# Performance work log

Hardware: AMD Instinct MI355X
Metric: run time of the kernel (lower is better)

The kernel has to match this reference:

```python
import jax, jax.numpy as jnp
import numpy as np
import math

D_MODEL = 1024
NUM_HEADS = 16
D_K = D_MODEL // NUM_HEADS


def setup_inputs() -> dict:
    key = jax.random.key(0)
    ks = jax.random.split(key, 5)
    scale = 1.0 / math.sqrt(D_MODEL)
    x = jax.random.normal(ks[0], (2, 2048, D_MODEL), dtype=jnp.float32)
    qkv_w = jax.random.uniform(ks[1], (3 * D_MODEL, D_MODEL), jnp.float32, -scale, scale)
    qkv_b = jax.random.uniform(ks[2], (3 * D_MODEL,), jnp.float32, -scale, scale)
    out_w = jax.random.uniform(ks[3], (D_MODEL, D_MODEL), jnp.float32, -scale, scale)
    out_b = jax.random.uniform(ks[4], (D_MODEL,), jnp.float32, -scale, scale)
    return {"x": x, "qkv_w": qkv_w, "qkv_b": qkv_b, "out_w": out_w, "out_b": out_b}


def reference(x, qkv_w, qkv_b, out_w, out_b):
    B, N, D = x.shape
    # fused QKV projection (torch Linear: x @ W.T + b)
    qkv = x @ qkv_w.T + qkv_b                       # (B, N, 3D)
    qkv = qkv.reshape(B, N, 3, NUM_HEADS, D_K)
    qkv = jnp.transpose(qkv, (2, 0, 3, 1, 4))        # (3, B, H, N, d_k)
    q, k, v = qkv[0], qkv[1], qkv[2]
    attn = jnp.einsum('bhnd,bhmd->bhnm', q, k) / math.sqrt(D_K)  # (B,H,N,N)
    attn = jax.nn.softmax(attn, axis=-1)
    out = jnp.einsum('bhnm,bhmd->bhnd', attn, v)     # (B,H,N,d_k)
    out = jnp.transpose(out, (0, 2, 1, 3)).reshape(B, N, D)
    return out @ out_w.T + out_b
```

## Files before the change

### kernel.cpp

```cpp
#include <hip/hip_runtime.h>
#include <hip/hip_bf16.h>


typedef __bf16 bf16x8 __attribute__((ext_vector_type(8)));
typedef __bf16 bf16x4 __attribute__((ext_vector_type(4)));
typedef short short4v __attribute__((ext_vector_type(4)));
typedef float f32x4 __attribute__((ext_vector_type(4)));

#define QSCALE 0.18033688011112042f

__device__ __forceinline__ unsigned short bfbits(float f) {
    union { __bf16 h; unsigned short u; } cv;
    cv.h = (__bf16)f;
    return cv.u;
}

__device__ __forceinline__ f32x4 mfma16(bf16x4 a, bf16x4 b, f32x4 c) {
#if __has_builtin(__builtin_amdgcn_mfma_f32_16x16x16bf16_1k)
    union { bf16x4 h; short4v s; } ua, ub;
    ua.h = a; ub.h = b;
    return __builtin_amdgcn_mfma_f32_16x16x16bf16_1k(ua.s, ub.s, c, 0, 0, 0);
#else
    f32x4 d = c;
    asm volatile("v_mfma_f32_16x16x16_bf16 %0, %1, %2, %0"
                 : "+v"(d) : "v"(a), "v"(b));
    return d;
#endif
}

__device__ __forceinline__ void gl_lds16(const void* g, void* l) {
    __builtin_amdgcn_global_load_lds(
        (__attribute__((address_space(1))) const unsigned int*)g,
        (__attribute__((address_space(3))) unsigned int*)l, 16, 0, 0);
}

__global__ void cvt_f32_bf16_v4(const float4* __restrict__ src,
                                ushort4* __restrict__ dst, int n4) {
    int i = blockIdx.x * blockDim.x + threadIdx.x;
    int stride = gridDim.x * blockDim.x;
    for (; i < n4; i += stride) {
        float4 f = src[i];
        ushort4 o;
        o.x = bfbits(f.x); o.y = bfbits(f.y); o.z = bfbits(f.z); o.w = bfbits(f.w);
        dst[i] = o;
    }
}

template<int MODE>
__global__ __launch_bounds__(256, 3) void gemm_mfma(
    const unsigned short* __restrict__ A,
    const unsigned short* __restrict__ W,
    const float* __restrict__ bias,
    unsigned short* __restrict__ qo,
    unsigned short* __restrict__ ko,
    unsigned short* __restrict__ vto,
    float* __restrict__ fo) {
    __shared__ __attribute__((aligned(128))) unsigned char smem[32768];
    const int lane = threadIdx.x & 63;
    const int w = threadIdx.x >> 6;
    const int g = lane >> 4, c = lane & 15;
    const int wr = w >> 1, wc = w & 1;
    const int row0 = blockIdx.x * 128;
    const int col0 = blockIdx.y * 128;

    const int rloc = lane >> 3;
    const int csrc = ((lane & 7) ^ rloc) * 8;

    f32x4 acc[4][4] = {};

    for (int kt = 0; kt < 1024; kt += 64) {
        #pragma unroll
        for (int i = 0; i < 4; ++i) {
            const int r = i * 32 + w * 8 + rloc;
            gl_lds16(A + (size_t)(row0 + r) * 1024 + kt + csrc,
                     smem + i * 4096 + w * 1024);
            gl_lds16(W + (size_t)(col0 + r) * 1024 + kt + csrc,
                     smem + 16384 + i * 4096 + w * 1024);
        }
        __syncthreads();

        #pragma unroll
        for (int ks = 0; ks < 2; ++ks) {
            bf16x8 a[4], b[4];
            #pragma unroll
            for (int mi = 0; mi < 4; ++mi) {
                const int r = wr * 64 + mi * 16 + c;
                a[mi] = *(const bf16x8*)(smem + r * 128 + (((ks * 4 + g) ^ (r & 7)) * 16));
            }
            #pragma unroll
            for (int ni = 0; ni < 4; ++ni) {
                const int r = wc * 64 + ni * 16 + c;
                b[ni] = *(const bf16x8*)(smem + 16384 + r * 128 + (((ks * 4 + g) ^ (r & 7)) * 16));
            }
            #pragma unroll
            for (int mi = 0; mi < 4; ++mi)
                #pragma unroll
                for (int ni = 0; ni < 4; ++ni)
                    acc[mi][ni] = __builtin_amdgcn_mfma_f32_16x16x32_bf16(
                        a[mi], b[ni], acc[mi][ni], 0, 0, 0);
        }
        __syncthreads();
    }

    #pragma unroll
    for (int mi = 0; mi < 4; ++mi) {
        #pragma unroll
        for (int ni = 0; ni < 4; ++ni) {
            const int col = col0 + wc * 64 + ni * 16 + c;
            const float bv = bias[col];
            #pragma unroll
            for (int j = 0; j < 4; ++j) {
                const int row = row0 + wr * 64 + mi * 16 + 4 * g + j;
                float v = acc[mi][ni][j] + bv;
                if (MODE == 1) {
                    fo[(size_t)row * 1024 + col] = v;
                } else {
                    const int sec = col >> 10;
                    const int d = col & 1023;
                    const int h = d >> 6, dk = d & 63;
                    const int b_ = row >> 11, n = row & 2047;
                    const int bh = b_ * 16 + h;
                    if (sec == 0)
                        qo[((size_t)(bh * 2048 + n) << 6) + dk] = bfbits(v * QSCALE);
                    else if (sec == 1)
                        ko[((size_t)(bh * 2048 + n) << 6) + dk] = bfbits(v);
                    else
                        vto[(size_t)(bh * 64 + dk) * 2048 + n] = bfbits(v);
                }
            }
        }
    }
}

__global__ __launch_bounds__(256, 4) void attn_flash(
    const unsigned short* __restrict__ Q,
    const unsigned short* __restrict__ K,
    const unsigned short* __restrict__ Vt,
    unsigned short* __restrict__ O) {
    __shared__ __attribute__((aligned(128))) unsigned char smem[32768];
    const int lane = threadIdx.x & 63;
    const int w = threadIdx.x >> 6;
    const int g = lane >> 4, c = lane & 15;
    const int c7 = c & 7;
    const int bh = blockIdx.y;
    const int q0 = blockIdx.x * 64 + w * 16;
    const unsigned short* Qb = Q + (size_t)bh * 2048 * 64;
    const unsigned short* Kb = K + (size_t)bh * 2048 * 64;
    const unsigned short* Vb = Vt + (size_t)bh * 64 * 2048;

    const int rloc = lane >> 3;
    const int csrc = ((lane & 7) ^ (rloc & 7)) * 8;

    const int chunkKV0 = ((0 + g) ^ c7) * 16;
    const int chunkKV1 = ((4 + g) ^ c7) * 16;
    const int ghalf = (g >> 1);
    const int gsub = (g & 1) * 8;

    bf16x8 aq[2];
    #pragma unroll
    for (int ks = 0; ks < 2; ++ks)
        aq[ks] = *(const bf16x8*)(Qb + (size_t)(q0 + c) * 64 + ks * 32 + 8 * g);

    f32x4 o[4] = {};
    f32x4 l_run = {};
    float m_run = -1e30f;

    bf16x4 ones4;
    #pragma unroll
    for (int i = 0; i < 4; ++i) ones4[i] = (__bf16)1.0f;

    #pragma unroll
    for (int tt = 0; tt < 2; ++tt) {
        const int t = 2 * w + tt;
        const int row = 8 * t + rloc;
        gl_lds16(Kb + (size_t)row * 64 + csrc, smem + t * 1024);
        gl_lds16(Vb + (size_t)row * 2048 + csrc, smem + 16384 + t * 1024);
    }
    __syncthreads();

    int cur = 0;
    for (int kv = 0; kv < 2048; kv += 64) {
        if (kv + 64 < 2048) {
            const int nb = cur ^ 1;
            #pragma unroll
            for (int tt = 0; tt < 2; ++tt) {
                const int t = 2 * w + tt;
                const int row = 8 * t + rloc;
                gl_lds16(Kb + (size_t)(kv + 64 + row) * 64 + csrc,
                         smem + nb * 8192 + t * 1024);
                gl_lds16(Vb + (size_t)row * 2048 + (kv + 64) + csrc,
                         smem + 16384 + nb * 8192 + t * 1024);
            }
        }

        const unsigned char* Kt = smem + cur * 8192;
        const unsigned char* Vtb = smem + 16384 + cur * 8192;

        f32x4 s[4] = {};
        __builtin_amdgcn_s_setprio(1);
        #pragma unroll
        for (int nj = 0; nj < 4; ++nj) {
            bf16x8 bk0 = *(const bf16x8*)(Kt + nj * 2048 + c * 128 + chunkKV0);
            bf16x8 bk1 = *(const bf16x8*)(Kt + nj * 2048 + c * 128 + chunkKV1);
            s[nj] = __builtin_amdgcn_mfma_f32_16x16x32_bf16(bk0, aq[0], s[nj], 0, 0, 0);
            s[nj] = __builtin_amdgcn_mfma_f32_16x16x32_bf16(bk1, aq[1], s[nj], 0, 0, 0);
        }
        __builtin_amdgcn_s_setprio(0);

        float pmax = s[0][0];
        #pragma unroll
        for (int nj = 0; nj < 4; ++nj)
            #pragma unroll
            for (int j = 0; j < 4; ++j)
                pmax = fmaxf(pmax, s[nj][j]);

        if (__any((int)(pmax > m_run + 8.f))) {
            float rm = pmax;
            rm = fmaxf(rm, __shfl_xor(rm, 16));
            rm = fmaxf(rm, __shfl_xor(rm, 32));
            const float mnew = fmaxf(m_run, rm);
            const float sc = __builtin_amdgcn_exp2f(m_run - mnew);
            m_run = mnew;
            #pragma unroll
            for (int j = 0; j < 4; ++j) {
                const float scj = __shfl(sc, 4 * g + j);
                l_run[j] *= scj;
                #pragma unroll
                for (int ni = 0; ni < 4; ++ni)
                    o[ni][j] *= scj;
            }
        }

        bf16x4 p[4];
        #pragma unroll
        for (int nj = 0; nj < 4; ++nj)
            #pragma unroll
            for (int j = 0; j < 4; ++j)
                p[nj][j] = (__bf16)__builtin_amdgcn_exp2f(s[nj][j] - m_run);

        f32x4 lt = {};
        __builtin_amdgcn_s_setprio(1);
        #pragma unroll
        for (int nj = 0; nj < 4; ++nj) {
            lt = mfma16(p[nj], ones4, lt);
            #pragma unroll
            for (int ni = 0; ni < 4; ++ni) {
                bf16x4 bv = *(const bf16x4*)(Vtb + (ni * 16 + c) * 128 +
                                             (((2 * nj + ghalf) ^ c7) * 16) + gsub);
                o[ni] = mfma16(p[nj], bv, o[ni]);
            }
        }
        __builtin_amdgcn_s_setprio(0);
        l_run += lt;

        __syncthreads();
        cur ^= 1;
    }

    const int b_ = bh >> 4, h = bh & 15;
    #pragma unroll
    for (int ni = 0; ni < 4; ++ni) {
        #pragma unroll
        for (int j = 0; j < 4; ++j) {
            const int row = b_ * 2048 + q0 + 4 * g + j;
            const int col = h * 64 + ni * 16 + c;
            O[(size_t)row * 1024 + col] = bfbits(o[ni][j] / l_run[j]);
        }
    }
}

extern "C" void kernel_launch(void* const* d_in, const int* in_sizes, int n_in,
                              void* d_out, int out_size, void* d_ws, size_t ws_size,
                              hipStream_t stream) {
    const float* x     = (const float*)d_in[0];
    const float* qkv_w = (const float*)d_in[1];
    const float* qkv_b = (const float*)d_in[2];
    const float* out_w = (const float*)d_in[3];
    const float* out_b = (const float*)d_in[4];
    float* out = (float*)d_out;

    char* ws = (char*)d_ws;
    unsigned short* xb   = (unsigned short*)(ws);
    unsigned short* wqkv = (unsigned short*)(ws + (8u  << 20));
    unsigned short* wout = (unsigned short*)(ws + (14u << 20));
    unsigned short* qb   = (unsigned short*)(ws + (16u << 20));
    unsigned short* kb   = (unsigned short*)(ws + (24u << 20));
    unsigned short* vtb  = (unsigned short*)(ws + (32u << 20));

    cvt_f32_bf16_v4<<<2048, 256, 0, stream>>>((const float4*)x,     (ushort4*)xb,   4096 * 1024 / 4);
    cvt_f32_bf16_v4<<<2048, 256, 0, stream>>>((const float4*)qkv_w, (ushort4*)wqkv, 3072 * 1024 / 4);
    cvt_f32_bf16_v4<<<1024, 256, 0, stream>>>((const float4*)out_w, (ushort4*)wout, 1024 * 1024 / 4);

    gemm_mfma<0><<<dim3(32, 24), 256, 0, stream>>>(xb, wqkv, qkv_b, qb, kb, vtb, nullptr);

    unsigned short* ao = xb;
    attn_flash<<<dim3(32, 32), 256, 0, stream>>>(qb, kb, vtb, ao);

    gemm_mfma<1><<<dim3(32, 8), 256, 0, stream>>>(ao, wout, out_b, nullptr, nullptr, nullptr, out);
}
```

Before: 130.7 us.

## Process two query groups per wave in attention and merge conversion kernels

Each attention wave now computes 32 query rows as two 16-row groups that share every K and V fragment read from LDS. Blocks shrink to 128 threads, and each thread issues twice the async tile loads. This halves LDS traffic per MFMA and amortizes the softmax bookkeeping, at the cost of higher register pressure and fewer waves per block. The three fp32-to-bf16 conversion launches are also merged into one kernel writing the contiguous workspace.

```diff
diff --git a/kernel.cpp b/kernel.cpp
--- a/kernel.cpp
+++ b/kernel.cpp
@@ -34,12 +34,17 @@
         (__attribute__((address_space(3))) unsigned int*)l, 16, 0, 0);
 }
 
-__global__ void cvt_f32_bf16_v4(const float4* __restrict__ src,
-                                ushort4* __restrict__ dst, int n4) {
+__global__ void cvt_all(const float4* __restrict__ x,
+                        const float4* __restrict__ wq,
+                        const float4* __restrict__ wo,
+                        ushort4* __restrict__ dst) {
     int i = blockIdx.x * blockDim.x + threadIdx.x;
-    int stride = gridDim.x * blockDim.x;
-    for (; i < n4; i += stride) {
-        float4 f = src[i];
+    const int stride = gridDim.x * blockDim.x;
+    for (; i < 2097152; i += stride) {
+        float4 f;
+        if (i < 1048576)       f = x[i];
+        else if (i < 1835008)  f = wq[i - 1048576];
+        else                   f = wo[i - 1835008];
         ushort4 o;
         o.x = bfbits(f.x); o.y = bfbits(f.y); o.z = bfbits(f.z); o.w = bfbits(f.w);
         dst[i] = o;
@@ -132,7 +137,7 @@
     }
 }
 
-__global__ __launch_bounds__(256, 4) void attn_flash(
+__global__ __launch_bounds__(128, 2) void attn_flash(
     const unsigned short* __restrict__ Q,
     const unsigned short* __restrict__ K,
     const unsigned short* __restrict__ Vt,
@@ -143,7 +148,7 @@
     const int g = lane >> 4, c = lane & 15;
     const int c7 = c & 7;
     const int bh = blockIdx.y;
-    const int q0 = blockIdx.x * 64 + w * 16;
+    const int q0 = blockIdx.x * 64 + w * 32;
     const unsigned short* Qb = Q + (size_t)bh * 2048 * 64;
     const unsigned short* Kb = K + (size_t)bh * 2048 * 64;
     const unsigned short* Vb = Vt + (size_t)bh * 64 * 2048;
@@ -156,22 +161,24 @@
     const int ghalf = (g >> 1);
     const int gsub = (g & 1) * 8;
 
-    bf16x8 aq[2];
-    #pragma unroll
-    for (int ks = 0; ks < 2; ++ks)
-        aq[ks] = *(const bf16x8*)(Qb + (size_t)(q0 + c) * 64 + ks * 32 + 8 * g);
-
-    f32x4 o[4] = {};
-    f32x4 l_run = {};
-    float m_run = -1e30f;
+    bf16x8 aq[2][2];
+    #pragma unroll
+    for (int qg = 0; qg < 2; ++qg)
+        #pragma unroll
+        for (int ks = 0; ks < 2; ++ks)
+            aq[qg][ks] = *(const bf16x8*)(Qb + (size_t)(q0 + qg * 16 + c) * 64 + ks * 32 + 8 * g);
+
+    f32x4 oa[4] = {}, ob[4] = {};
+    f32x4 la = {}, lb = {};
+    float ma = -1e30f, mb = -1e30f;
 
     bf16x4 ones4;
     #pragma unroll
     for (int i = 0; i < 4; ++i) ones4[i] = (__bf16)1.0f;
 
     #pragma unroll
-    for (int tt = 0; tt < 2; ++tt) {
-        const int t = 2 * w + tt;
+    for (int tt = 0; tt < 4; ++tt) {
+        const int t = 4 * w + tt;
         const int row = 8 * t + rloc;
         gl_lds16(Kb + (size_t)row * 64 + csrc, smem + t * 1024);
         gl_lds16(Vb + (size_t)row * 2048 + csrc, smem + 16384 + t * 1024);
@@ -183,8 +190,8 @@
         if (kv + 64 < 2048) {
             const int nb = cur ^ 1;
             #pragma unroll
-            for (int tt = 0; tt < 2; ++tt) {
-                const int t = 2 * w + tt;
+            for (int tt = 0; tt < 4; ++tt) {
+                const int t = 4 * w + tt;
                 const int row = 8 * t + rloc;
                 gl_lds16(Kb + (size_t)(kv + 64 + row) * 64 + csrc,
                          smem + nb * 8192 + t * 1024);
@@ -196,62 +203,84 @@
         const unsigned char* Kt = smem + cur * 8192;
         const unsigned char* Vtb = smem + 16384 + cur * 8192;
 
-        f32x4 s[4] = {};
+        f32x4 sa[4] = {}, sb[4] = {};
         __builtin_amdgcn_s_setprio(1);
         #pragma unroll
         for (int nj = 0; nj < 4; ++nj) {
             bf16x8 bk0 = *(const bf16x8*)(Kt + nj * 2048 + c * 128 + chunkKV0);
             bf16x8 bk1 = *(const bf16x8*)(Kt + nj * 2048 + c * 128 + chunkKV1);
-            s[nj] = __builtin_amdgcn_mfma_f32_16x16x32_bf16(bk0, aq[0], s[nj], 0, 0, 0);
-            s[nj] = __builtin_amdgcn_mfma_f32_16x16x32_bf16(bk1, aq[1], s[nj], 0, 0, 0);
+            sa[nj] = __builtin_amdgcn_mfma_f32_16x16x32_bf16(bk0, aq[0][0], sa[nj], 0, 0, 0);
+            sa[nj] = __builtin_amdgcn_mfma_f32_16x16x32_bf16(bk1, aq[0][1], sa[nj], 0, 0, 0);
+            sb[nj] = __builtin_amdgcn_mfma_f32_16x16x32_bf16(bk0, aq[1][0], sb[nj], 0, 0, 0);
+            sb[nj] = __builtin_amdgcn_mfma_f32_16x16x32_bf16(bk1, aq[1][1], sb[nj], 0, 0, 0);
         }
         __builtin_amdgcn_s_setprio(0);
 
-        float pmax = s[0][0];
+        float pa = sa[0][0], pb = sb[0][0];
         #pragma unroll
         for (int nj = 0; nj < 4; ++nj)
             #pragma unroll
-            for (int j = 0; j < 4; ++j)
-                pmax = fmaxf(pmax, s[nj][j]);
-
-        if (__any((int)(pmax > m_run + 8.f))) {
-            float rm = pmax;
+            for (int j = 0; j < 4; ++j) {
+                pa = fmaxf(pa, sa[nj][j]);
+                pb = fmaxf(pb, sb[nj][j]);
+            }
+
+        const bool trig = (pa > ma + 8.f) || (pb > mb + 8.f);
+        if (__any((int)trig)) {
+            float rm = pa;
             rm = fmaxf(rm, __shfl_xor(rm, 16));
             rm = fmaxf(rm, __shfl_xor(rm, 32));
-            const float mnew = fmaxf(m_run, rm);
-            const float sc = __builtin_amdgcn_exp2f(m_run - mnew);
-            m_run = mnew;
+            float mnew = fmaxf(ma, rm);
+            float sc = __builtin_amdgcn_exp2f(ma - mnew);
+            ma = mnew;
             #pragma unroll
             for (int j = 0; j < 4; ++j) {
                 const float scj = __shfl(sc, 4 * g + j);
-                l_run[j] *= scj;
+                la[j] *= scj;
                 #pragma unroll
-                for (int ni = 0; ni < 4; ++ni)
-                    o[ni][j] *= scj;
-            }
-        }
-
-        bf16x4 p[4];
+                for (int ni = 0; ni < 4; ++ni) oa[ni][j] *= scj;
+            }
+            rm = pb;
+            rm = fmaxf(rm, __shfl_xor(rm, 16));
+            rm = fmaxf(rm, __shfl_xor(rm, 32));
+            mnew = fmaxf(mb, rm);
+            sc = __builtin_amdgcn_exp2f(mb - mnew);
+            mb = mnew;
+            #pragma unroll
+            for (int j = 0; j < 4; ++j) {
+                const float scj = __shfl(sc, 4 * g + j);
+                lb[j] *= scj;
+                #pragma unroll
+                for (int ni = 0; ni < 4; ++ni) ob[ni][j] *= scj;
+            }
+        }
+
+        bf16x4 qa_[4], qb_[4];
         #pragma unroll
         for (int nj = 0; nj < 4; ++nj)
             #pragma unroll
-            for (int j = 0; j < 4; ++j)
-                p[nj][j] = (__bf16)__builtin_amdgcn_exp2f(s[nj][j] - m_run);
-
-        f32x4 lt = {};
+            for (int j = 0; j < 4; ++j) {
+                qa_[nj][j] = (__bf16)__builtin_amdgcn_exp2f(sa[nj][j] - ma);
+                qb_[nj][j] = (__bf16)__builtin_amdgcn_exp2f(sb[nj][j] - mb);
+            }
+
+        f32x4 lta = {}, ltb = {};
         __builtin_amdgcn_s_setprio(1);
         #pragma unroll
         for (int nj = 0; nj < 4; ++nj) {
-            lt = mfma16(p[nj], ones4, lt);
+            lta = mfma16(qa_[nj], ones4, lta);
+            ltb = mfma16(qb_[nj], ones4, ltb);
             #pragma unroll
             for (int ni = 0; ni < 4; ++ni) {
                 bf16x4 bv = *(const bf16x4*)(Vtb + (ni * 16 + c) * 128 +
                                              (((2 * nj + ghalf) ^ c7) * 16) + gsub);
-                o[ni] = mfma16(p[nj], bv, o[ni]);
+                oa[ni] = mfma16(qa_[nj], bv, oa[ni]);
+                ob[ni] = mfma16(qb_[nj], bv, ob[ni]);
             }
         }
         __builtin_amdgcn_s_setprio(0);
-        l_run += lt;
+        la += lta;
+        lb += ltb;
 
         __syncthreads();
         cur ^= 1;
@@ -262,9 +291,11 @@
     for (int ni = 0; ni < 4; ++ni) {
         #pragma unroll
         for (int j = 0; j < 4; ++j) {
-            const int row = b_ * 2048 + q0 + 4 * g + j;
             const int col = h * 64 + ni * 16 + c;
-            O[(size_t)row * 1024 + col] = bfbits(o[ni][j] / l_run[j]);
+            const int rowa = b_ * 2048 + q0 + 4 * g + j;
+            O[(size_t)rowa * 1024 + col] = bfbits(oa[ni][j] / la[j]);
+            const int rowb = rowa + 16;
+            O[(size_t)rowb * 1024 + col] = bfbits(ob[ni][j] / lb[j]);
         }
     }
 }
@@ -287,14 +318,13 @@
     unsigned short* kb   = (unsigned short*)(ws + (24u << 20));
     unsigned short* vtb  = (unsigned short*)(ws + (32u << 20));
 
-    cvt_f32_bf16_v4<<<2048, 256, 0, stream>>>((const float4*)x,     (ushort4*)xb,   4096 * 1024 / 4);
-    cvt_f32_bf16_v4<<<2048, 256, 0, stream>>>((const float4*)qkv_w, (ushort4*)wqkv, 3072 * 1024 / 4);
-    cvt_f32_bf16_v4<<<1024, 256, 0, stream>>>((const float4*)out_w, (ushort4*)wout, 1024 * 1024 / 4);
+    cvt_all<<<2048, 256, 0, stream>>>((const float4*)x, (const float4*)qkv_w,
+                                      (const float4*)out_w, (ushort4*)ws);
 
     gemm_mfma<0><<<dim3(32, 24), 256, 0, stream>>>(xb, wqkv, qkv_b, qb, kb, vtb, nullptr);
 
     unsigned short* ao = xb;
-    attn_flash<<<dim3(32, 32), 256, 0, stream>>>(qb, kb, vtb, ao);
+    attn_flash<<<dim3(32, 32), 128, 0, stream>>>(qb, kb, vtb, ao);
 
     gemm_mfma<1><<<dim3(32, 8), 256, 0, stream>>>(ao, wout, out_b, nullptr, nullptr, nullptr, out);
 }
```

Measured after the change: 130.5 us. About the same (-0.2%).

## Software-pipeline attention QK^T with softmax/PV and merge conversion kernels

Applied to the files above, without the earlier changes.

The flash-attention loop is restructured so that the QK^T MFMAs for the next KV tile are issued before the softmax and PV work on the current tile. It uses two score register sets, double-buffered K and triple-buffered V in LDS, which grows LDS from 32 KB to 40 KB. This aims to hide MFMA latency behind the exp/max work and overlap loads further ahead. The three f32-to-bf16 conversion launches are also merged into one kernel over the contiguous workspace, which relies on the fixed buffer offsets.

```diff
diff --git a/kernel.cpp b/kernel.cpp
--- a/kernel.cpp
+++ b/kernel.cpp
@@ -34,12 +34,17 @@
         (__attribute__((address_space(3))) unsigned int*)l, 16, 0, 0);
 }
 
-__global__ void cvt_f32_bf16_v4(const float4* __restrict__ src,
-                                ushort4* __restrict__ dst, int n4) {
+__global__ void cvt_all(const float4* __restrict__ x,
+                        const float4* __restrict__ wq,
+                        const float4* __restrict__ wo,
+                        ushort4* __restrict__ dst) {
     int i = blockIdx.x * blockDim.x + threadIdx.x;
-    int stride = gridDim.x * blockDim.x;
-    for (; i < n4; i += stride) {
-        float4 f = src[i];
+    const int stride = gridDim.x * blockDim.x;
+    for (; i < 2097152; i += stride) {
+        float4 f;
+        if (i < 1048576)       f = x[i];
+        else if (i < 1835008)  f = wq[i - 1048576];
+        else                   f = wo[i - 1835008];
         ushort4 o;
         o.x = bfbits(f.x); o.y = bfbits(f.y); o.z = bfbits(f.z); o.w = bfbits(f.w);
         dst[i] = o;
@@ -137,7 +142,7 @@
     const unsigned short* __restrict__ K,
     const unsigned short* __restrict__ Vt,
     unsigned short* __restrict__ O) {
-    __shared__ __attribute__((aligned(128))) unsigned char smem[32768];
+    __shared__ __attribute__((aligned(128))) unsigned char smem[40960];
     const int lane = threadIdx.x & 63;
     const int w = threadIdx.x >> 6;
     const int g = lane >> 4, c = lane & 15;
@@ -169,93 +174,108 @@
     #pragma unroll
     for (int i = 0; i < 4; ++i) ones4[i] = (__bf16)1.0f;
 
-    #pragma unroll
-    for (int tt = 0; tt < 2; ++tt) {
-        const int t = 2 * w + tt;
-        const int row = 8 * t + rloc;
-        gl_lds16(Kb + (size_t)row * 64 + csrc, smem + t * 1024);
-        gl_lds16(Vb + (size_t)row * 2048 + csrc, smem + 16384 + t * 1024);
-    }
+    #define STAGE(U, KBUF, VBUF)                                               \
+        {                                                                      \
+            _Pragma("unroll")                                                  \
+            for (int tt = 0; tt < 2; ++tt) {                                   \
+                const int t = 2 * w + tt;                                      \
+                const int row = 8 * t + rloc;                                  \
+                gl_lds16(Kb + (size_t)((U) * 64 + row) * 64 + csrc,            \
+                         smem + (KBUF) * 8192 + t * 1024);                     \
+                gl_lds16(Vb + (size_t)row * 2048 + (U) * 64 + csrc,            \
+                         smem + 16384 + (VBUF) * 8192 + t * 1024);             \
+            }                                                                  \
+        }
+
+    #define QKT(S, KBUF)                                                       \
+        {                                                                      \
+            const unsigned char* Kt = smem + (KBUF) * 8192;                    \
+            __builtin_amdgcn_s_setprio(1);                                     \
+            _Pragma("unroll")                                                  \
+            for (int nj = 0; nj < 4; ++nj) {                                   \
+                bf16x8 bk0 = *(const bf16x8*)(Kt + nj * 2048 + c * 128 + chunkKV0); \
+                bf16x8 bk1 = *(const bf16x8*)(Kt + nj * 2048 + c * 128 + chunkKV1); \
+                S[nj] = __builtin_amdgcn_mfma_f32_16x16x32_bf16(bk0, aq[0], S[nj], 0, 0, 0); \
+                S[nj] = __builtin_amdgcn_mfma_f32_16x16x32_bf16(bk1, aq[1], S[nj], 0, 0, 0); \
+            }                                                                  \
+            __builtin_amdgcn_s_setprio(0);                                     \
+        }
+
+    #define SMPV(S, VBUF)                                                      \
+        {                                                                      \
+            float pmax = S[0][0];                                              \
+            _Pragma("unroll")                                                  \
+            for (int nj = 0; nj < 4; ++nj)                                     \
+                _Pragma("unroll")                                              \
+                for (int j = 0; j < 4; ++j)                                    \
+                    pmax = fmaxf(pmax, S[nj][j]);                              \
+            if (__any((int)(pmax > m_run + 8.f))) {                            \
+                float rm = pmax;                                               \
+                rm = fmaxf(rm, __shfl_xor(rm, 16));                            \
+                rm = fmaxf(rm, __shfl_xor(rm, 32));                            \
+                const float mnew = fmaxf(m_run, rm);                           \
+                const float sc = __builtin_amdgcn_exp2f(m_run - mnew);         \
+                m_run = mnew;                                                  \
+                _Pragma("unroll")                                              \
+                for (int j = 0; j < 4; ++j) {                                  \
+                    const float scj = __shfl(sc, 4 * g + j);                   \
+                    l_run[j] *= scj;                                           \
+                    _Pragma("unroll")                                          \
+                    for (int ni = 0; ni < 4; ++ni) o[ni][j] *= scj;            \
+                }                                                              \
+            }                                                                  \
+            bf16x4 p[4];                                                       \
+            _Pragma("unroll")                                                  \
+            for (int nj = 0; nj < 4; ++nj)                                     \
+                _Pragma("unroll")                                              \
+                for (int j = 0; j < 4; ++j)                                    \
+                    p[nj][j] = (__bf16)__builtin_amdgcn_exp2f(S[nj][j] - m_run); \
+            const unsigned char* Vtb = smem + 16384 + (VBUF) * 8192;           \
+            f32x4 lt = {};                                                     \
+            __builtin_amdgcn_s_setprio(1);                                     \
+            _Pragma("unroll")                                                  \
+            for (int nj = 0; nj < 4; ++nj) {                                   \
+                lt = mfma16(p[nj], ones4, lt);                                 \
+                _Pragma("unroll")                                              \
+                for (int ni = 0; ni < 4; ++ni) {                               \
+                    bf16x4 bv = *(const bf16x4*)(Vtb + (ni * 16 + c) * 128 +   \
+                                 (((2 * nj + ghalf) ^ c7) * 16) + gsub);       \
+                    o[ni] = mfma16(p[nj], bv, o[ni]);                          \
+                }                                                              \
+            }                                                                  \
+            __builtin_amdgcn_s_setprio(0);                                     \
+            l_run += lt;                                                       \
+        }
+
+    f32x4 sA[4] = {}, sB[4] = {};
+
+    STAGE(0, 0, 0);
     __syncthreads();
-
-    int cur = 0;
-    for (int kv = 0; kv < 2048; kv += 64) {
-        if (kv + 64 < 2048) {
-            const int nb = cur ^ 1;
-            #pragma unroll
-            for (int tt = 0; tt < 2; ++tt) {
-                const int t = 2 * w + tt;
-                const int row = 8 * t + rloc;
-                gl_lds16(Kb + (size_t)(kv + 64 + row) * 64 + csrc,
-                         smem + nb * 8192 + t * 1024);
-                gl_lds16(Vb + (size_t)row * 2048 + (kv + 64) + csrc,
-                         smem + 16384 + nb * 8192 + t * 1024);
-            }
-        }
-
-        const unsigned char* Kt = smem + cur * 8192;
-        const unsigned char* Vtb = smem + 16384 + cur * 8192;
-
-        f32x4 s[4] = {};
-        __builtin_amdgcn_s_setprio(1);
-        #pragma unroll
-        for (int nj = 0; nj < 4; ++nj) {
-            bf16x8 bk0 = *(const bf16x8*)(Kt + nj * 2048 + c * 128 + chunkKV0);
-            bf16x8 bk1 = *(const bf16x8*)(Kt + nj * 2048 + c * 128 + chunkKV1);
-            s[nj] = __builtin_amdgcn_mfma_f32_16x16x32_bf16(bk0, aq[0], s[nj], 0, 0, 0);
-            s[nj] = __builtin_amdgcn_mfma_f32_16x16x32_bf16(bk1, aq[1], s[nj], 0, 0, 0);
-        }
-        __builtin_amdgcn_s_setprio(0);
-
-        float pmax = s[0][0];
-        #pragma unroll
-        for (int nj = 0; nj < 4; ++nj)
-            #pragma unroll
-            for (int j = 0; j < 4; ++j)
-                pmax = fmaxf(pmax, s[nj][j]);
-
-        if (__any((int)(pmax > m_run + 8.f))) {
-            float rm = pmax;
-            rm = fmaxf(rm, __shfl_xor(rm, 16));
-            rm = fmaxf(rm, __shfl_xor(rm, 32));
-            const float mnew = fmaxf(m_run, rm);
-            const float sc = __builtin_amdgcn_exp2f(m_run - mnew);
-            m_run = mnew;
-            #pragma unroll
-            for (int j = 0; j < 4; ++j) {
-                const float scj = __shfl(sc, 4 * g + j);
-                l_run[j] *= scj;
-                #pragma unroll
-                for (int ni = 0; ni < 4; ++ni)
-                    o[ni][j] *= scj;
-            }
-        }
-
-        bf16x4 p[4];
-        #pragma unroll
-        for (int nj = 0; nj < 4; ++nj)
-            #pragma unroll
-            for (int j = 0; j < 4; ++j)
-                p[nj][j] = (__bf16)__builtin_amdgcn_exp2f(s[nj][j] - m_run);
-
-        f32x4 lt = {};
-        __builtin_amdgcn_s_setprio(1);
-        #pragma unroll
-        for (int nj = 0; nj < 4; ++nj) {
-            lt = mfma16(p[nj], ones4, lt);
-            #pragma unroll
-            for (int ni = 0; ni < 4; ++ni) {
-                bf16x4 bv = *(const bf16x4*)(Vtb + (ni * 16 + c) * 128 +
-                                             (((2 * nj + ghalf) ^ c7) * 16) + gsub);
-                o[ni] = mfma16(p[nj], bv, o[ni]);
-            }
-        }
-        __builtin_amdgcn_s_setprio(0);
-        l_run += lt;
-
+    STAGE(1, 1, 1);
+    QKT(sA, 0);
+    __syncthreads();
+
+    for (int u = 1; u < 31; u += 2) {
+        STAGE(u + 1, 0, (u + 1) % 3);
+        QKT(sB, 1);
+        SMPV(sA, (u - 1) % 3);
         __syncthreads();
-        cur ^= 1;
-    }
+        #pragma unroll
+        for (int nj = 0; nj < 4; ++nj) sA[nj] = f32x4{};
+        STAGE(u + 2, 1, (u + 2) % 3);
+        QKT(sA, 0);
+        SMPV(sB, u % 3);
+        __syncthreads();
+        #pragma unroll
+        for (int nj = 0; nj < 4; ++nj) sB[nj] = f32x4{};
+    }
+    QKT(sB, 1);
+    SMPV(sA, 0);
+    SMPV(sB, 1);
+
+    #undef STAGE
+    #undef QKT
+    #undef SMPV
 
     const int b_ = bh >> 4, h = bh & 15;
     #pragma unroll
@@ -287,9 +307,8 @@
     unsigned short* kb   = (unsigned short*)(ws + (24u << 20));
     unsigned short* vtb  = (unsigned short*)(ws + (32u << 20));
 
-    cvt_f32_bf16_v4<<<2048, 256, 0, stream>>>((const float4*)x,     (ushort4*)xb,   4096 * 1024 / 4);
-    cvt_f32_bf16_v4<<<2048, 256, 0, stream>>>((const float4*)qkv_w, (ushort4*)wqkv, 3072 * 1024 / 4);
-    cvt_f32_bf16_v4<<<1024, 256, 0, stream>>>((const float4*)out_w, (ushort4*)wout, 1024 * 1024 / 4);
+    cvt_all<<<2048, 256, 0, stream>>>((const float4*)x, (const float4*)qkv_w,
+                                      (const float4*)out_w, (ushort4*)ws);
 
     gemm_mfma<0><<<dim3(32, 24), 256, 0, stream>>>(xb, wqkv, qkv_b, qb, kb, vtb, nullptr);
 
```

Result: faster. 127.6 us (-2.3%).

## Widen attention blocks to 128 queries sharing K/V tiles; merge conversion kernels

Applied to the files above, without the earlier changes.

The flash attention kernel now runs 8 waves (512 threads) per block over 128 query rows, so each 64-row K/V tile staged in LDS serves twice as many queries. This halves global K/V traffic and the number of blocks. Each wave now loads one 1 KB chunk per tile, and the LDS XOR swizzle folds in row bit 3 to keep reads conflict-free. The three f32-to-bf16 conversion launches are merged into one kernel writing the contiguous workspace, trading launch overhead for a per-element branch. Larger blocks also mean coarser barriers across 8 waves and a tighter register budget under the new launch bounds.

```diff
diff --git a/kernel.cpp b/kernel.cpp
--- a/kernel.cpp
+++ b/kernel.cpp
@@ -34,12 +34,17 @@
         (__attribute__((address_space(3))) unsigned int*)l, 16, 0, 0);
 }
 
-__global__ void cvt_f32_bf16_v4(const float4* __restrict__ src,
-                                ushort4* __restrict__ dst, int n4) {
+__global__ void cvt_all(const float4* __restrict__ x,
+                        const float4* __restrict__ wq,
+                        const float4* __restrict__ wo,
+                        ushort4* __restrict__ dst) {
     int i = blockIdx.x * blockDim.x + threadIdx.x;
-    int stride = gridDim.x * blockDim.x;
-    for (; i < n4; i += stride) {
-        float4 f = src[i];
+    const int stride = gridDim.x * blockDim.x;
+    for (; i < 2097152; i += stride) {
+        float4 f;
+        if (i < 1048576)       f = x[i];
+        else if (i < 1835008)  f = wq[i - 1048576];
+        else                   f = wo[i - 1835008];
         ushort4 o;
         o.x = bfbits(f.x); o.y = bfbits(f.y); o.z = bfbits(f.z); o.w = bfbits(f.w);
         dst[i] = o;
@@ -132,7 +137,7 @@
     }
 }
 
-__global__ __launch_bounds__(256, 4) void attn_flash(
+__global__ __launch_bounds__(512, 8) void attn_flash(
     const unsigned short* __restrict__ Q,
     const unsigned short* __restrict__ K,
     const unsigned short* __restrict__ Vt,
@@ -142,18 +147,19 @@
     const int w = threadIdx.x >> 6;
     const int g = lane >> 4, c = lane & 15;
     const int c7 = c & 7;
+    const int swz = c7 ^ (((c >> 3) & 1) << 2);
     const int bh = blockIdx.y;
-    const int q0 = blockIdx.x * 64 + w * 16;
+    const int q0 = blockIdx.x * 128 + w * 16;
     const unsigned short* Qb = Q + (size_t)bh * 2048 * 64;
     const unsigned short* Kb = K + (size_t)bh * 2048 * 64;
     const unsigned short* Vb = Vt + (size_t)bh * 64 * 2048;
 
     const int rloc = lane >> 3;
-    const int csrc = ((lane & 7) ^ (rloc & 7)) * 8;
-
-    const int chunkKV0 = ((0 + g) ^ c7) * 16;
-    const int chunkKV1 = ((4 + g) ^ c7) * 16;
-    const int ghalf = (g >> 1);
+    const int csrc = ((lane & 7) ^ rloc ^ ((w & 1) << 2)) * 8;
+
+    const int chunkKV0 = ((0 + g) ^ swz) * 16;
+    const int chunkKV1 = ((4 + g) ^ swz) * 16;
+    const int ghalf = g >> 1;
     const int gsub = (g & 1) * 8;
 
     bf16x8 aq[2];
@@ -169,28 +175,22 @@
     #pragma unroll
     for (int i = 0; i < 4; ++i) ones4[i] = (__bf16)1.0f;
 
-    #pragma unroll
-    for (int tt = 0; tt < 2; ++tt) {
-        const int t = 2 * w + tt;
-        const int row = 8 * t + rloc;
-        gl_lds16(Kb + (size_t)row * 64 + csrc, smem + t * 1024);
-        gl_lds16(Vb + (size_t)row * 2048 + csrc, smem + 16384 + t * 1024);
+    {
+        const int row = 8 * w + rloc;
+        gl_lds16(Kb + (size_t)row * 64 + csrc, smem + w * 1024);
+        gl_lds16(Vb + (size_t)row * 2048 + csrc, smem + 16384 + w * 1024);
     }
     __syncthreads();
 
-    int cur = 0;
-    for (int kv = 0; kv < 2048; kv += 64) {
-        if (kv + 64 < 2048) {
+    for (int t = 0; t < 32; ++t) {
+        const int cur = t & 1;
+        if (t + 1 < 32) {
             const int nb = cur ^ 1;
-            #pragma unroll
-            for (int tt = 0; tt < 2; ++tt) {
-                const int t = 2 * w + tt;
-                const int row = 8 * t + rloc;
-                gl_lds16(Kb + (size_t)(kv + 64 + row) * 64 + csrc,
-                         smem + nb * 8192 + t * 1024);
-                gl_lds16(Vb + (size_t)row * 2048 + (kv + 64) + csrc,
-                         smem + 16384 + nb * 8192 + t * 1024);
-            }
+            const int row = 8 * w + rloc;
+            gl_lds16(Kb + (size_t)((t + 1) * 64 + row) * 64 + csrc,
+                     smem + nb * 8192 + w * 1024);
+            gl_lds16(Vb + (size_t)row * 2048 + (t + 1) * 64 + csrc,
+                     smem + 16384 + nb * 8192 + w * 1024);
         }
 
         const unsigned char* Kt = smem + cur * 8192;
@@ -226,8 +226,7 @@
                 const float scj = __shfl(sc, 4 * g + j);
                 l_run[j] *= scj;
                 #pragma unroll
-                for (int ni = 0; ni < 4; ++ni)
-                    o[ni][j] *= scj;
+                for (int ni = 0; ni < 4; ++ni) o[ni][j] *= scj;
             }
         }
 
@@ -246,7 +245,7 @@
             #pragma unroll
             for (int ni = 0; ni < 4; ++ni) {
                 bf16x4 bv = *(const bf16x4*)(Vtb + (ni * 16 + c) * 128 +
-                                             (((2 * nj + ghalf) ^ c7) * 16) + gsub);
+                                             (((2 * nj + ghalf) ^ swz) * 16) + gsub);
                 o[ni] = mfma16(p[nj], bv, o[ni]);
             }
         }
@@ -254,7 +253,6 @@
         l_run += lt;
 
         __syncthreads();
-        cur ^= 1;
     }
 
     const int b_ = bh >> 4, h = bh & 15;
@@ -287,14 +285,13 @@
     unsigned short* kb   = (unsigned short*)(ws + (24u << 20));
     unsigned short* vtb  = (unsigned short*)(ws + (32u << 20));
 
-    cvt_f32_bf16_v4<<<2048, 256, 0, stream>>>((const float4*)x,     (ushort4*)xb,   4096 * 1024 / 4);
-    cvt_f32_bf16_v4<<<2048, 256, 0, stream>>>((const float4*)qkv_w, (ushort4*)wqkv, 3072 * 1024 / 4);
-    cvt_f32_bf16_v4<<<1024, 256, 0, stream>>>((const float4*)out_w, (ushort4*)wout, 1024 * 1024 / 4);
+    cvt_all<<<2048, 256, 0, stream>>>((const float4*)x, (const float4*)qkv_w,
+                                      (const float4*)out_w, (ushort4*)ws);
 
     gemm_mfma<0><<<dim3(32, 24), 256, 0, stream>>>(xb, wqkv, qkv_b, qb, kb, vtb, nullptr);
 
     unsigned short* ao = xb;
-    attn_flash<<<dim3(32, 32), 256, 0, stream>>>(qb, kb, vtb, ao);
+    attn_flash<<<dim3(16, 32), 512, 0, stream>>>(qb, kb, vtb, ao);
 
     gemm_mfma<1><<<dim3(32, 8), 256, 0, stream>>>(ao, wout, out_b, nullptr, nullptr, nullptr, out);
 }
```

New measurement: 126.1 us. 3.5% less time.
